# Optimization experiments

Measured on AMD Instinct MI355X. Metric: run time of the kernel, lower is better.

Reference implementation:

```python
import jax, jax.numpy as jnp
import numpy as np

B, S, D, H = 2, 2048, 1024, 16
HD = D // H  # 64
EPS = 1e-8


def setup_inputs() -> dict:
    key = jax.random.key(0)
    ks = jax.random.split(key, 9)
    hidden_states = jax.random.normal(ks[0], (B, S, D), dtype=jnp.float32)
    # rotary tables: standard RoPE angles over half the head dim
    pos = jnp.arange(S, dtype=jnp.float32)[:, None]
    inv_freq = 1.0 / (10000.0 ** (jnp.arange(0, HD, 2, dtype=jnp.float32) / HD))  # [HD/2]
    ang = pos * inv_freq[None, :]  # [S, HD/2]
    sin = jnp.sin(ang)[None, None]  # [1,1,S,HD/2]
    cos = jnp.cos(ang)[None, None]
    s = 1.0 / np.sqrt(D)
    wq = jax.random.normal(ks[1], (D, D), dtype=jnp.float32) * s
    wk = jax.random.normal(ks[2], (D, D), dtype=jnp.float32) * s
    wv = jax.random.normal(ks[3], (D, D), dtype=jnp.float32) * s
    wo = jax.random.normal(ks[4], (D, D), dtype=jnp.float32) * s
    bo = jnp.zeros((D,), dtype=jnp.float32)
    scale = jnp.ones((D,), dtype=jnp.float32)
    return {"hidden_states": hidden_states, "sin": sin, "cos": cos,
            "wq": wq, "wk": wk, "wv": wv, "wo": wo, "bo": bo, "scale": scale}


def _heads(x):
    # [B,S,D] -> [B,H,S,HD]
    return x.reshape(B, S, H, HD).transpose(0, 2, 1, 3)


def _rotary(x, sin, cos):
    # interleaved RoPE: even/odd pairs
    x1, x2 = x[..., 0::2], x[..., 1::2]
    out = jnp.stack([x1 * cos - x2 * sin, x2 * cos + x1 * sin], axis=-1)
    return out.reshape(x.shape)


def reference(hidden_states, sin, cos, wq, wk, wv, wo, bo, scale):
    q = _rotary(_heads(hidden_states @ wq.T), sin, cos)
    k = _rotary(_heads(hidden_states @ wk.T), sin, cos)
    v = _rotary(_heads(hidden_states @ wv.T), sin, cos)
    scores = jnp.einsum("bhqd,bhkd->bhqk", q, k) / np.sqrt(HD)
    probs = jax.nn.softmax(scores, axis=-1)
    ctx = jnp.einsum("bhqk,bhkd->bhqd", probs, v)
    ctx = ctx.transpose(0, 2, 1, 3).reshape(B, S, D)
    out = ctx @ wo.T + bo
    x = out + hidden_states
    # RMSNorm: x / (||x||/sqrt(d) + eps) * scale
    rms = jnp.linalg.norm(x, axis=-1, keepdims=True) / np.sqrt(D)
    return scale * (x / (rms + EPS))
```

## Files before the change

### kernel.cpp

```cpp
#include <hip/hip_runtime.h>
#include <cmath>

#define BB 2
#define SS 2048
#define DD 1024
#define HH 16
#define HDIM 64
#define KDIM 1024
#define EPSF 1e-8f
#define QSCALE 0.18033688f

typedef __attribute__((ext_vector_type(8))) short bf16x8;
typedef __attribute__((ext_vector_type(4))) float f32x4;
typedef __attribute__((ext_vector_type(16))) float f32x16;

__device__ __forceinline__ ushort f2bf(float x) {
    unsigned u = __builtin_bit_cast(unsigned, x);
    u += 0x7FFFu + ((u >> 16) & 1u);
    return (ushort)(u >> 16);
}

__device__ __forceinline__ unsigned pack_bf16_trunc(float a, float b) {
    return __builtin_amdgcn_perm(__builtin_bit_cast(unsigned, b),
                                 __builtin_bit_cast(unsigned, a), 0x07060302u);
}

__device__ __forceinline__ void gload_lds16(const ushort* g, ushort* l) {
    __builtin_amdgcn_global_load_lds(
        (const __attribute__((address_space(1))) unsigned*)g,
        (__attribute__((address_space(3))) unsigned*)l, 16, 0, 0);
}

__global__ __launch_bounds__(256) void conv_all(
    const float* __restrict__ hs, const float* __restrict__ wq,
    const float* __restrict__ wk, const float* __restrict__ wv,
    const float* __restrict__ wo, ushort* __restrict__ dst)
{
    const int i = blockIdx.x * 256 + threadIdx.x;
    const int HS4 = (BB * SS * DD) / 4;
    const int W4 = (DD * DD) / 4;
    const float* src;
    int off;
    if (i < HS4) { src = hs; off = i; }
    else {
        const int j = i - HS4;
        const int seg = j / W4;
        off = j - seg * W4;
        src = (seg == 0) ? wq : (seg == 1) ? wk : (seg == 2) ? wv : wo;
    }
    const float4 v = ((const float4*)src)[off];
    ushort4 o;
    o.x = f2bf(v.x); o.y = f2bf(v.y); o.z = f2bf(v.z); o.w = f2bf(v.w);
    ((ushort4*)dst)[i] = o;
}

__global__ __launch_bounds__(256) void gemm_qkv_mfma(
    const ushort* __restrict__ A,
    const ushort* __restrict__ Wq, const ushort* __restrict__ Wk,
    const ushort* __restrict__ Wv,
    const float* __restrict__ sinp, const float* __restrict__ cosp,
    ushort* __restrict__ Qb, ushort* __restrict__ Kb, ushort* __restrict__ Vtb)
{
    const int cb = blockIdx.y;
    const int z = cb >> 3;
    const int col0 = (cb & 7) * 128;
    const ushort* W = (z == 0) ? Wq : (z == 1) ? Wk : Wv;
    ushort* O = (z == 0) ? Qb : (z == 1) ? Kb : Vtb;
    const int row0 = blockIdx.x * 128;
    const float qs = (z == 0) ? QSCALE : 1.0f;

    __shared__ __align__(16) ushort As[128 * 32];
    __shared__ __align__(16) ushort Bs[128 * 32];

    const int tid = threadIdx.x;
    const int w = tid >> 6, lane = tid & 63;
    const int quad = lane >> 4, l15 = lane & 15;
    const int m_off = (w >> 1) * 64, n_off = (w & 1) * 64;

    f32x4 acc[4][4] = {};

    for (int k0 = 0; k0 < KDIM; k0 += 32) {
#pragma unroll
        for (int it = 0; it < 2; ++it) {
            const int L = (it * 4 + w) * 64 + lane;
            const int r = L >> 2, c8 = (L & 3) * 8;
            gload_lds16(A + (size_t)(row0 + r) * KDIM + k0 + c8, &As[L * 8]);
            gload_lds16(W + (size_t)(col0 + r) * KDIM + k0 + c8, &Bs[L * 8]);
        }
        __syncthreads();
        bf16x8 af[4], bfr[4];
#pragma unroll
        for (int i = 0; i < 4; ++i) {
            af[i]  = *(const bf16x8*)&As[(m_off + i * 16 + l15) * 32 + quad * 8];
            bfr[i] = *(const bf16x8*)&Bs[(n_off + i * 16 + l15) * 32 + quad * 8];
        }
#pragma unroll
        for (int i = 0; i < 4; ++i)
#pragma unroll
            for (int j = 0; j < 4; ++j)
                acc[i][j] = __builtin_amdgcn_mfma_f32_16x16x32_bf16(
                    af[i], bfr[j], acc[i][j], 0, 0, 0);
        __syncthreads();
    }

    const int b = (row0 + m_off) / SS;
#pragma unroll
    for (int mi = 0; mi < 4; ++mi) {
        const int mrow = row0 + m_off + mi * 16 + quad * 4;
#pragma unroll
        for (int ni = 0; ni < 4; ++ni) {
            const int c = col0 + n_off + ni * 16 + l15;
            const int h = c >> 6, e = c & 63;
            const int bh = b * HH + h;
            float outv[4];
#pragma unroll
            for (int r = 0; r < 4; ++r) {
                const int s = (mrow + r) & (SS - 1);
                const float sv = sinp[s * (HDIM / 2) + (e >> 1)];
                const float cv = cosp[s * (HDIM / 2) + (e >> 1)];
                const float v = acc[mi][ni][r];
                const float vp = __shfl_xor(v, 1);
                outv[r] = ((l15 & 1) ? (v * cv + vp * sv) : (v * cv - vp * sv)) * qs;
            }
            if (z < 2) {
#pragma unroll
                for (int r = 0; r < 4; ++r) {
                    const int s = (mrow + r) & (SS - 1);
                    const ushort mine = f2bf(outv[r]);
                    const ushort part = (ushort)__shfl_xor((int)mine, 1);
                    if (!(l15 & 1))
                        *(unsigned*)(O + ((size_t)(bh * SS + s)) * HDIM + e) =
                            (unsigned)mine | ((unsigned)part << 16);
                }
            } else {
                ushort4 pk;
                pk.x = f2bf(outv[0]); pk.y = f2bf(outv[1]);
                pk.z = f2bf(outv[2]); pk.w = f2bf(outv[3]);
                const int s0 = mrow & (SS - 1);
                *(ushort4*)(O + ((size_t)(bh * HDIM + e)) * SS + s0) = pk;
            }
        }
    }
}

__global__ __launch_bounds__(256) void attn_mfma(
    const ushort* __restrict__ Qb, const ushort* __restrict__ Kb,
    const ushort* __restrict__ Vtb, ushort* __restrict__ ctx)
{
    const int bh = blockIdx.y;
    const int b = bh / HH, h = bh % HH;
    const int q0 = blockIdx.x * 128;
    const int tid = threadIdx.x;
    const int w = tid >> 6;
    const int lane = tid & 63;
    const int l31 = lane & 31;
    const int g = lane >> 5;

    __shared__ __align__(16) ushort klds[4096];
    __shared__ __align__(16) ushort vlds[4096];

    const ushort* Qh = Qb  + (size_t)bh * SS * HDIM;
    const ushort* Kh = Kb  + (size_t)bh * SS * HDIM;
    const ushort* Vh = Vtb + (size_t)bh * HDIM * SS;

    const int qrow = q0 + w * 32 + l31;
    bf16x8 qf[4];
#pragma unroll
    for (int ks = 0; ks < 4; ++ks)
        qf[ks] = *(const bf16x8*)(Qh + (size_t)qrow * HDIM + ks * 16 + g * 8);

    f32x16 cacc[2] = {};
    float lsum = 0.f;

    const int lr = lane >> 2;
    const int lc = (lane & 3) * 8;

    union U32x4 { unsigned u[4]; bf16x8 v; };

    for (int k0 = 0; k0 < SS; k0 += 64) {
#pragma unroll
        for (int hf = 0; hf < 2; ++hf) {
            gload_lds16(Kh + (size_t)(k0 + w * 16 + lr) * HDIM + hf * 32 + lc,
                        &klds[(hf * 64 + w * 16 + lr) * 32 + lc]);
            gload_lds16(Vh + (size_t)(w * 16 + lr) * SS + k0 + hf * 32 + lc,
                        &vlds[(hf * 64 + w * 16 + lr) * 32 + lc]);
        }
        __syncthreads();

        f32x16 sacc[2] = {};
#pragma unroll
        for (int kt = 0; kt < 2; ++kt)
#pragma unroll
            for (int ks = 0; ks < 4; ++ks) {
                const bf16x8 kf = *(const bf16x8*)&klds[
                    ((ks >> 1) * 64 + kt * 32 + l31) * 32 + (ks & 1) * 16 + g * 8];
                sacc[kt] = __builtin_amdgcn_mfma_f32_32x32x16_bf16(
                    kf, qf[ks], sacc[kt], 0, 0, 0);
            }

        unsigned pk[2][8];
#pragma unroll
        for (int kt = 0; kt < 2; ++kt)
#pragma unroll
            for (int i = 0; i < 8; ++i) {
                const float pa = exp2f(sacc[kt][2 * i]);
                const float pb = exp2f(sacc[kt][2 * i + 1]);
                lsum += pa + pb;
                pk[kt][i] = pack_bf16_trunc(pa, pb);
            }

#pragma unroll
        for (int ks = 0; ks < 4; ++ks) {
            const int kt = ks >> 1, bq = (ks & 1) * 4;
            const unsigned s0 = (unsigned)__shfl_xor((int)pk[kt][bq + 0], 32);
            const unsigned s1 = (unsigned)__shfl_xor((int)pk[kt][bq + 1], 32);
            const unsigned s2 = (unsigned)__shfl_xor((int)pk[kt][bq + 2], 32);
            const unsigned s3 = (unsigned)__shfl_xor((int)pk[kt][bq + 3], 32);
            U32x4 pf;
            pf.u[0] = g ? s2 : pk[kt][bq + 0];
            pf.u[1] = g ? s3 : pk[kt][bq + 1];
            pf.u[2] = g ? pk[kt][bq + 2] : s0;
            pf.u[3] = g ? pk[kt][bq + 3] : s1;
#pragma unroll
            for (int dt = 0; dt < 2; ++dt) {
                const bf16x8 vf = *(const bf16x8*)&vlds[
                    ((ks >> 1) * 64 + dt * 32 + l31) * 32 + (ks & 1) * 16 + g * 8];
                cacc[dt] = __builtin_amdgcn_mfma_f32_32x32x16_bf16(
                    vf, pf.v, cacc[dt], 0, 0, 0);
            }
        }
        __syncthreads();
    }

    lsum += __shfl_xor(lsum, 32);
    const float inv = 1.f / lsum;

    const size_t obase = ((size_t)(b * SS + qrow)) * DD + h * HDIM;
#pragma unroll
    for (int dt = 0; dt < 2; ++dt)
#pragma unroll
        for (int t = 0; t < 4; ++t) {
            ushort4 o;
            o.x = f2bf(cacc[dt][t * 4 + 0] * inv);
            o.y = f2bf(cacc[dt][t * 4 + 1] * inv);
            o.z = f2bf(cacc[dt][t * 4 + 2] * inv);
            o.w = f2bf(cacc[dt][t * 4 + 3] * inv);
            *(ushort4*)(ctx + obase + dt * 32 + t * 8 + g * 4) = o;
        }
}

__global__ __launch_bounds__(256) void gemm_out_mfma(
    const ushort* __restrict__ A, const ushort* __restrict__ W,
    const float* __restrict__ bias, float* __restrict__ Out)
{
    const int row0 = blockIdx.x * 128;
    const int col0 = blockIdx.y * 128;

    __shared__ __align__(16) ushort As[128 * 32];
    __shared__ __align__(16) ushort Bs[128 * 32];

    const int tid = threadIdx.x;
    const int w = tid >> 6, lane = tid & 63;
    const int quad = lane >> 4, l15 = lane & 15;
    const int m_off = (w >> 1) * 64, n_off = (w & 1) * 64;

    f32x4 acc[4][4] = {};

    for (int k0 = 0; k0 < KDIM; k0 += 32) {
#pragma unroll
        for (int it = 0; it < 2; ++it) {
            const int L = (it * 4 + w) * 64 + lane;
            const int r = L >> 2, c8 = (L & 3) * 8;
            gload_lds16(A + (size_t)(row0 + r) * KDIM + k0 + c8, &As[L * 8]);
            gload_lds16(W + (size_t)(col0 + r) * KDIM + k0 + c8, &Bs[L * 8]);
        }
        __syncthreads();
        bf16x8 af[4], bfr[4];
#pragma unroll
        for (int i = 0; i < 4; ++i) {
            af[i]  = *(const bf16x8*)&As[(m_off + i * 16 + l15) * 32 + quad * 8];
            bfr[i] = *(const bf16x8*)&Bs[(n_off + i * 16 + l15) * 32 + quad * 8];
        }
#pragma unroll
        for (int i = 0; i < 4; ++i)
#pragma unroll
            for (int j = 0; j < 4; ++j)
                acc[i][j] = __builtin_amdgcn_mfma_f32_16x16x32_bf16(
                    af[i], bfr[j], acc[i][j], 0, 0, 0);
        __syncthreads();
    }

#pragma unroll
    for (int mi = 0; mi < 4; ++mi) {
        const int mrow = row0 + m_off + mi * 16 + quad * 4;
#pragma unroll
        for (int ni = 0; ni < 4; ++ni) {
            const int c = col0 + n_off + ni * 16 + l15;
            const float bv = bias[c];
#pragma unroll
            for (int r = 0; r < 4; ++r)
                Out[(size_t)(mrow + r) * DD + c] = acc[mi][ni][r] + bv;
        }
    }
}

__global__ __launch_bounds__(256) void resid_rmsnorm(
    const float* __restrict__ proj, const float* __restrict__ hs,
    const float* __restrict__ scale, float* __restrict__ out)
{
    const int t = blockIdx.x;
    const int tid = threadIdx.x;
    const size_t base = (size_t)t * DD + tid * 4;

    const float4 p4 = *(const float4*)(proj + base);
    const float4 h4 = *(const float4*)(hs + base);
    float x0 = p4.x + h4.x, x1 = p4.y + h4.y, x2 = p4.z + h4.z, x3 = p4.w + h4.w;
    float ss = x0 * x0 + x1 * x1 + x2 * x2 + x3 * x3;

#pragma unroll
    for (int off = 1; off < 64; off <<= 1) ss += __shfl_xor(ss, off);

    __shared__ float wsum[4];
    if ((tid & 63) == 0) wsum[tid >> 6] = ss;
    __syncthreads();
    const float total = wsum[0] + wsum[1] + wsum[2] + wsum[3];
    const float inv = 1.f / (sqrtf(total * (1.f / DD)) + EPSF);

    const float4 s4 = *(const float4*)(scale + tid * 4);
    float4 o;
    o.x = s4.x * x0 * inv;
    o.y = s4.y * x1 * inv;
    o.z = s4.z * x2 * inv;
    o.w = s4.w * x3 * inv;
    *(float4*)(out + base) = o;
}

extern "C" void kernel_launch(void* const* d_in, const int* in_sizes, int n_in,
                              void* d_out, int out_size, void* d_ws, size_t ws_size,
                              hipStream_t stream) {
    const float* hs    = (const float*)d_in[0];
    const float* sinp  = (const float*)d_in[1];
    const float* cosp  = (const float*)d_in[2];
    const float* wq    = (const float*)d_in[3];
    const float* wk    = (const float*)d_in[4];
    const float* wv    = (const float*)d_in[5];
    const float* wo    = (const float*)d_in[6];
    const float* bo    = (const float*)d_in[7];
    const float* scale = (const float*)d_in[8];
    float* out = (float*)d_out;

    unsigned char* wsb = (unsigned char*)d_ws;
    const size_t MAT = (size_t)BB * SS * DD;
    const size_t WN  = (size_t)DD * DD;
    ushort* Abf = (ushort*)wsb;
    ushort* Wqb = Abf + MAT;
    ushort* Wkb = Wqb + WN;
    ushort* Wvb = Wkb + WN;
    ushort* Wob = Wvb + WN;
    ushort* Qb  = Wob + WN;
    ushort* Kb  = Qb + MAT;
    ushort* Vtb = Kb + MAT;
    ushort* ctxb = Vtb + MAT;
    float* proj = (float*)(ctxb + MAT);

    const int nconv4 = (int)((MAT + 4 * WN) / 4);
    conv_all<<<dim3(nconv4 / 256), 256, 0, stream>>>(hs, wq, wk, wv, wo, Abf);

    gemm_qkv_mfma<<<dim3(32, 24), 256, 0, stream>>>(Abf, Wqb, Wkb, Wvb,
                                                    sinp, cosp, Qb, Kb, Vtb);
    attn_mfma<<<dim3(SS / 128, BB * HH), 256, 0, stream>>>(Qb, Kb, Vtb, ctxb);
    gemm_out_mfma<<<dim3(32, 8), 256, 0, stream>>>(ctxb, Wob, bo, proj);
    resid_rmsnorm<<<dim3(BB * SS), 256, 0, stream>>>(proj, hs, scale, out);
}
```

Measured before the change: 230.1 us.

## Split attention keys across wave pairs, shrink out-proj tiles, use raw v_exp

The attention kernel now gives each 32-query strip to two waves. Each wave handles alternate 64-key blocks from a 128-key LDS stage, and the partial accumulators and row sums are merged through LDS at the end. This doubles the block count from 512 to 1024 to improve occupancy and CU fill. The output-projection GEMM tile drops from 128x128 to 128x64, doubling its grid to 512 blocks for better load balance. exp2f is replaced by inline v_exp_f32 to avoid the range-handling wrapper. The costs are a final LDS reduction plus sync, more redundant A-tile loads in the GEMM, and less accurate exp2 on denormal inputs.

```diff
diff --git a/kernel.cpp b/kernel.cpp
--- a/kernel.cpp
+++ b/kernel.cpp
@@ -23,6 +23,12 @@
 __device__ __forceinline__ unsigned pack_bf16_trunc(float a, float b) {
     return __builtin_amdgcn_perm(__builtin_bit_cast(unsigned, b),
                                  __builtin_bit_cast(unsigned, a), 0x07060302u);
+}
+
+__device__ __forceinline__ float exp2_fast(float x) {
+    float r;
+    asm("v_exp_f32 %0, %1" : "=v"(r) : "v"(x));
+    return r;
 }
 
 __device__ __forceinline__ void gload_lds16(const ushort* g, ushort* l) {
@@ -149,21 +155,22 @@
 {
     const int bh = blockIdx.y;
     const int b = bh / HH, h = bh % HH;
-    const int q0 = blockIdx.x * 128;
+    const int q0 = blockIdx.x * 64;
     const int tid = threadIdx.x;
     const int w = tid >> 6;
     const int lane = tid & 63;
     const int l31 = lane & 31;
     const int g = lane >> 5;
-
-    __shared__ __align__(16) ushort klds[4096];
-    __shared__ __align__(16) ushort vlds[4096];
+    const int strip = w >> 1;
+    const int phase = w & 1;
+
+    __shared__ __align__(16) ushort lds[16384];
 
     const ushort* Qh = Qb  + (size_t)bh * SS * HDIM;
     const ushort* Kh = Kb  + (size_t)bh * SS * HDIM;
     const ushort* Vh = Vtb + (size_t)bh * HDIM * SS;
 
-    const int qrow = q0 + w * 32 + l31;
+    const int qrow = q0 + strip * 32 + l31;
     bf16x8 qf[4];
 #pragma unroll
     for (int ks = 0; ks < 4; ++ks)
@@ -175,15 +182,22 @@
     const int lr = lane >> 2;
     const int lc = (lane & 3) * 8;
 
+    ushort* mybuf = &lds[phase * 8192];
+
     union U32x4 { unsigned u[4]; bf16x8 v; };
 
-    for (int k0 = 0; k0 < SS; k0 += 64) {
-#pragma unroll
-        for (int hf = 0; hf < 2; ++hf) {
-            gload_lds16(Kh + (size_t)(k0 + w * 16 + lr) * HDIM + hf * 32 + lc,
-                        &klds[(hf * 64 + w * 16 + lr) * 32 + lc]);
-            gload_lds16(Vh + (size_t)(w * 16 + lr) * SS + k0 + hf * 32 + lc,
-                        &vlds[(hf * 64 + w * 16 + lr) * 32 + lc]);
+    for (int k0 = 0; k0 < SS; k0 += 128) {
+#pragma unroll
+        for (int bq = 0; bq < 2; ++bq) {
+            ushort* bufb = &lds[bq * 8192];
+            const int kb = k0 + bq * 64;
+#pragma unroll
+            for (int hf = 0; hf < 2; ++hf) {
+                gload_lds16(Kh + (size_t)(kb + w * 16 + lr) * HDIM + hf * 32 + lc,
+                            &bufb[(hf * 64 + w * 16 + lr) * 32 + lc]);
+                gload_lds16(Vh + (size_t)(w * 16 + lr) * SS + kb + hf * 32 + lc,
+                            &bufb[4096 + (hf * 64 + w * 16 + lr) * 32 + lc]);
+            }
         }
         __syncthreads();
 
@@ -192,7 +206,7 @@
         for (int kt = 0; kt < 2; ++kt)
 #pragma unroll
             for (int ks = 0; ks < 4; ++ks) {
-                const bf16x8 kf = *(const bf16x8*)&klds[
+                const bf16x8 kf = *(const bf16x8*)&mybuf[
                     ((ks >> 1) * 64 + kt * 32 + l31) * 32 + (ks & 1) * 16 + g * 8];
                 sacc[kt] = __builtin_amdgcn_mfma_f32_32x32x16_bf16(
                     kf, qf[ks], sacc[kt], 0, 0, 0);
@@ -203,8 +217,8 @@
         for (int kt = 0; kt < 2; ++kt)
 #pragma unroll
             for (int i = 0; i < 8; ++i) {
-                const float pa = exp2f(sacc[kt][2 * i]);
-                const float pb = exp2f(sacc[kt][2 * i + 1]);
+                const float pa = exp2_fast(sacc[kt][2 * i]);
+                const float pb = exp2_fast(sacc[kt][2 * i + 1]);
                 lsum += pa + pb;
                 pk[kt][i] = pack_bf16_trunc(pa, pb);
             }
@@ -223,8 +237,8 @@
             pf.u[3] = g ? pk[kt][bq + 3] : s1;
 #pragma unroll
             for (int dt = 0; dt < 2; ++dt) {
-                const bf16x8 vf = *(const bf16x8*)&vlds[
-                    ((ks >> 1) * 64 + dt * 32 + l31) * 32 + (ks & 1) * 16 + g * 8];
+                const bf16x8 vf = *(const bf16x8*)&mybuf[
+                    4096 + ((ks >> 1) * 64 + dt * 32 + l31) * 32 + (ks & 1) * 16 + g * 8];
                 cacc[dt] = __builtin_amdgcn_mfma_f32_32x32x16_bf16(
                     vf, pf.v, cacc[dt], 0, 0, 0);
             }
@@ -233,20 +247,38 @@
     }
 
     lsum += __shfl_xor(lsum, 32);
-    const float inv = 1.f / lsum;
-
-    const size_t obase = ((size_t)(b * SS + qrow)) * DD + h * HDIM;
-#pragma unroll
-    for (int dt = 0; dt < 2; ++dt)
-#pragma unroll
-        for (int t = 0; t < 4; ++t) {
-            ushort4 o;
-            o.x = f2bf(cacc[dt][t * 4 + 0] * inv);
-            o.y = f2bf(cacc[dt][t * 4 + 1] * inv);
-            o.z = f2bf(cacc[dt][t * 4 + 2] * inv);
-            o.w = f2bf(cacc[dt][t * 4 + 3] * inv);
-            *(ushort4*)(ctx + obase + dt * 32 + t * 8 + g * 4) = o;
-        }
+
+    float* mlds = (float*)lds;
+    const int mbase = strip * 2112 + lane * 33;
+    if (phase == 1) {
+#pragma unroll
+        for (int dt = 0; dt < 2; ++dt)
+#pragma unroll
+            for (int i = 0; i < 16; ++i) mlds[mbase + dt * 16 + i] = cacc[dt][i];
+        mlds[mbase + 32] = lsum;
+    }
+    __syncthreads();
+    if (phase == 0) {
+#pragma unroll
+        for (int dt = 0; dt < 2; ++dt)
+#pragma unroll
+            for (int i = 0; i < 16; ++i) cacc[dt][i] += mlds[mbase + dt * 16 + i];
+        lsum += mlds[mbase + 32];
+        const float inv = 1.f / lsum;
+
+        const size_t obase = ((size_t)(b * SS + qrow)) * DD + h * HDIM;
+#pragma unroll
+        for (int dt = 0; dt < 2; ++dt)
+#pragma unroll
+            for (int t = 0; t < 4; ++t) {
+                ushort4 o;
+                o.x = f2bf(cacc[dt][t * 4 + 0] * inv);
+                o.y = f2bf(cacc[dt][t * 4 + 1] * inv);
+                o.z = f2bf(cacc[dt][t * 4 + 2] * inv);
+                o.w = f2bf(cacc[dt][t * 4 + 3] * inv);
+                *(ushort4*)(ctx + obase + dt * 32 + t * 8 + g * 4) = o;
+            }
+    }
 }
 
 __global__ __launch_bounds__(256) void gemm_out_mfma(
@@ -254,17 +286,17 @@
     const float* __restrict__ bias, float* __restrict__ Out)
 {
     const int row0 = blockIdx.x * 128;
-    const int col0 = blockIdx.y * 128;
+    const int col0 = blockIdx.y * 64;
 
     __shared__ __align__(16) ushort As[128 * 32];
-    __shared__ __align__(16) ushort Bs[128 * 32];
+    __shared__ __align__(16) ushort Bs[64 * 32];
 
     const int tid = threadIdx.x;
     const int w = tid >> 6, lane = tid & 63;
     const int quad = lane >> 4, l15 = lane & 15;
-    const int m_off = (w >> 1) * 64, n_off = (w & 1) * 64;
-
-    f32x4 acc[4][4] = {};
+    const int m_off = (w >> 1) * 64, n_off = (w & 1) * 32;
+
+    f32x4 acc[4][2] = {};
 
     for (int k0 = 0; k0 < KDIM; k0 += 32) {
 #pragma unroll
@@ -272,19 +304,24 @@
             const int L = (it * 4 + w) * 64 + lane;
             const int r = L >> 2, c8 = (L & 3) * 8;
             gload_lds16(A + (size_t)(row0 + r) * KDIM + k0 + c8, &As[L * 8]);
+        }
+        {
+            const int L = w * 64 + lane;
+            const int r = L >> 2, c8 = (L & 3) * 8;
             gload_lds16(W + (size_t)(col0 + r) * KDIM + k0 + c8, &Bs[L * 8]);
         }
         __syncthreads();
-        bf16x8 af[4], bfr[4];
-#pragma unroll
-        for (int i = 0; i < 4; ++i) {
-            af[i]  = *(const bf16x8*)&As[(m_off + i * 16 + l15) * 32 + quad * 8];
-            bfr[i] = *(const bf16x8*)&Bs[(n_off + i * 16 + l15) * 32 + quad * 8];
-        }
+        bf16x8 af[4], bfr[2];
 #pragma unroll
         for (int i = 0; i < 4; ++i)
-#pragma unroll
-            for (int j = 0; j < 4; ++j)
+            af[i] = *(const bf16x8*)&As[(m_off + i * 16 + l15) * 32 + quad * 8];
+#pragma unroll
+        for (int j = 0; j < 2; ++j)
+            bfr[j] = *(const bf16x8*)&Bs[(n_off + j * 16 + l15) * 32 + quad * 8];
+#pragma unroll
+        for (int i = 0; i < 4; ++i)
+#pragma unroll
+            for (int j = 0; j < 2; ++j)
                 acc[i][j] = __builtin_amdgcn_mfma_f32_16x16x32_bf16(
                     af[i], bfr[j], acc[i][j], 0, 0, 0);
         __syncthreads();
@@ -294,7 +331,7 @@
     for (int mi = 0; mi < 4; ++mi) {
         const int mrow = row0 + m_off + mi * 16 + quad * 4;
 #pragma unroll
-        for (int ni = 0; ni < 4; ++ni) {
+        for (int ni = 0; ni < 2; ++ni) {
             const int c = col0 + n_off + ni * 16 + l15;
             const float bv = bias[c];
 #pragma unroll
@@ -368,7 +405,7 @@
 
     gemm_qkv_mfma<<<dim3(32, 24), 256, 0, stream>>>(Abf, Wqb, Wkb, Wvb,
                                                     sinp, cosp, Qb, Kb, Vtb);
-    attn_mfma<<<dim3(SS / 128, BB * HH), 256, 0, stream>>>(Qb, Kb, Vtb, ctxb);
-    gemm_out_mfma<<<dim3(32, 8), 256, 0, stream>>>(ctxb, Wob, bo, proj);
+    attn_mfma<<<dim3(SS / 64, BB * HH), 256, 0, stream>>>(Qb, Kb, Vtb, ctxb);
+    gemm_out_mfma<<<dim3(32, 16), 256, 0, stream>>>(ctxb, Wob, bo, proj);
     resid_rmsnorm<<<dim3(BB * SS), 256, 0, stream>>>(proj, hs, scale, out);
 }
```

Result: faster. 224.9 us (-2.3%).
